# Performance work log

Measured on AMD Instinct MI355X. Metric: run time of the kernel, lower is better.

Reference implementation:

```python
import jax, jax.numpy as jnp
import numpy as np

SQRT2 = 1.4142135623730951  # ScaleCostWeight(sqrt(2)) applied to residuals
N_ITERS = 10
DAMP = 1e-8  # tiny Tikhonov for numerical safety of the 6x6 solve


def _hat(phi):
    x, y, z = phi[0], phi[1], phi[2]
    o = jnp.zeros((), phi.dtype)
    return jnp.stack([jnp.stack([o, -z, y]),
                      jnp.stack([z, o, -x]),
                      jnp.stack([-y, x, o])])


def se3_exp(xi):
    # xi: [6] = [rho (trans), phi (rot)] -> 4x4 SE3 matrix
    rho, phi = xi[:3], xi[3:]
    theta2 = jnp.sum(phi * phi)
    small = theta2 < 1e-12
    theta2s = jnp.where(small, 1.0, theta2)  # double-where for safe grads
    theta = jnp.sqrt(theta2s)
    A = jnp.where(small, 1.0, jnp.sin(theta) / theta)
    B = jnp.where(small, 0.5, (1.0 - jnp.cos(theta)) / theta2s)
    C = jnp.where(small, 1.0 / 6.0, (theta - jnp.sin(theta)) / (theta2s * theta))
    K = _hat(phi)
    K2 = K @ K
    I3 = jnp.eye(3, dtype=xi.dtype)
    R = I3 + A * K + B * K2
    V = I3 + B * K + C * K2
    t = V @ rho
    top = jnp.concatenate([R, t[:, None]], axis=1)
    bot = jnp.array([[0.0, 0.0, 0.0, 1.0]], dtype=xi.dtype)
    return jnp.concatenate([top, bot], axis=0)


def se3_inv(T):
    R = T[..., :3, :3]
    t = T[..., :3, 3:]
    Rt = jnp.swapaxes(R, -1, -2)
    top = jnp.concatenate([Rt, -(Rt @ t)], axis=-1)
    bot = jnp.broadcast_to(jnp.array([0.0, 0.0, 0.0, 1.0], T.dtype),
                           T.shape[:-2] + (1, 4))
    return jnp.concatenate([top, bot], axis=-2)


def _r_single(xi, T, src3, trg3, Wh, w):
    # residual of one batch element at local perturbation xi (retract on right)
    Tn = T @ se3_exp(xi)
    pred = Tn[:3, :3] @ src3 + Tn[:3, 3:4]          # [3, N]
    e = trg3 - pred                                  # [3, N]
    ew = jnp.einsum('nij,jn->in', Wh, e) * w         # cholesky-weighted, w: [1,N]
    return (ew * SQRT2).reshape(-1)                  # [3N]


def _forward(src4, trg4, w, T_init, inv_cov, T_s_v):
    src3 = src4[:, :3, :]
    trg3 = trg4[:, :3, :]
    # W_half = cholesky(inv_cov)^T, computed once (aux var, constant over iters)
    Wh = jnp.swapaxes(jnp.linalg.cholesky(inv_cov), -1, -2)  # [B, N, 3, 3]
    B = src4.shape[0]
    I6 = jnp.eye(6, dtype=src4.dtype)

    def step(T, _):
        xi0 = jnp.zeros((B, 6), T.dtype)
        J = jax.vmap(jax.jacfwd(_r_single), in_axes=(0, 0, 0, 0, 0, 0))(
            xi0, T, src3, trg3, Wh, w)               # [B, 3N, 6]
        r = jax.vmap(_r_single)(xi0, T, src3, trg3, Wh, w)  # [B, 3N]
        g = jnp.einsum('bri,br->bi', J, r)
        H = jnp.einsum('bri,brj->bij', J, J) + DAMP * I6
        dx = -jnp.linalg.solve(H, g[..., None])[..., 0]
        return T @ jax.vmap(se3_exp)(dx), None

    T, _ = jax.lax.scan(step, T_init, None, length=N_ITERS)
    T_sv = jnp.broadcast_to(T_s_v, (B, 4, 4))
    return se3_inv(T_sv) @ T @ T_sv


def setup_inputs() -> dict:
    key = jax.random.key(0)
    B, N = 256, 2048
    k1, k2, k3, k4, k5, k6 = jax.random.split(key, 6)
    src3 = 2.0 * jax.random.normal(k1, (B, 3, N), dtype=jnp.float32)
    # well-posed registration problem: trg = T_true * src + noise
    T_true = jax.vmap(se3_exp)(0.3 * jax.random.normal(k2, (B, 6), dtype=jnp.float32))
    trg3 = (jnp.einsum('bij,bjn->bin', T_true[:, :3, :3], src3)
            + T_true[:, :3, 3:4]
            + 0.01 * jax.random.normal(k3, (B, 3, N), dtype=jnp.float32))
    ones = jnp.ones((B, 1, N), dtype=jnp.float32)
    keypoints_3D_src = jnp.concatenate([src3, ones], axis=1)
    keypoints_3D_trg = jnp.concatenate([trg3, ones], axis=1)
    weights = jax.random.uniform(k4, (B, 1, N), dtype=jnp.float32,
                                 minval=0.1, maxval=1.0)
    A = 0.3 * jax.random.normal(k5, (B, N, 3, 3), dtype=jnp.float32)
    inv_cov_weights = A @ jnp.swapaxes(A, -1, -2) + jnp.eye(3, dtype=jnp.float32)
    T_trg_src_init = jax.vmap(se3_exp)(
        0.05 * jax.random.normal(k6, (B, 6), dtype=jnp.float32))
    T_s_v = se3_exp(jnp.array([0.1, -0.2, 0.3, 0.2, -0.1, 0.15], dtype=jnp.float32))
    return {"keypoints_3D_src": keypoints_3D_src,
            "keypoints_3D_trg": keypoints_3D_trg,
            "weights": weights,
            "T_trg_src_init": T_trg_src_init,
            "inv_cov_weights": inv_cov_weights,
            "T_s_v": T_s_v}


def reference(keypoints_3D_src, keypoints_3D_trg, weights, T_trg_src_init,
              inv_cov_weights, T_s_v):
    return _forward(keypoints_3D_src, keypoints_3D_trg, weights,
                    T_trg_src_init, inv_cov_weights, T_s_v)
```

## Files before the change

kernel.cpp:

```cpp
#include <hip/hip_runtime.h>
#include <math.h>

#define NPTS   2048
#define BD1    256
#define PPT    (NPTS / BD1)
#define NMOM   72
#define NITERS 10
#define DAMPF  1e-8f

__launch_bounds__(BD1, 1)
__global__ void moments_kernel(const float* __restrict__ src4,
                               const float* __restrict__ trg4,
                               const float* __restrict__ wts,
                               const float* __restrict__ icov,
                               float* __restrict__ mom, int B)
{
    const int b   = blockIdx.x;
    const int tid = threadIdx.x;

    const float* srcb = src4 + (size_t)b * 4 * NPTS;
    const float* trgb = trg4 + (size_t)b * 4 * NPTS;
    const float* wb   = wts  + (size_t)b * NPTS;
    const float* cb   = icov + (size_t)b * NPTS * 9;

    float acc[NMOM];
    #pragma unroll
    for (int k = 0; k < NMOM; ++k) acc[k] = 0.0f;

    #pragma unroll
    for (int kk = 0; kk < PPT; ++kk) {
        int n = tid + kk * BD1;
        float sx = srcb[n], sy = srcb[NPTS + n], sz = srcb[2 * NPTS + n];
        float gx = trgb[n], gy = trgb[NPTS + n], gz = trgb[2 * NPTS + n];
        float w  = wb[n];
        const float* c = cb + (size_t)n * 9;
        float w2 = 2.0f * w * w;
        float W[6];
        W[0] = w2 * c[0];
        W[1] = w2 * c[3];
        W[2] = w2 * c[6];
        W[3] = w2 * c[4];
        W[4] = w2 * c[7];
        W[5] = w2 * c[8];

        float hx = W[0] * gx + W[1] * gy + W[2] * gz;
        float hy = W[1] * gx + W[3] * gy + W[4] * gz;
        float hz = W[2] * gx + W[4] * gy + W[5] * gz;

        float sv[3] = { sx, sy, sz };
        float hv[3] = { hx, hy, hz };
        float ss[6] = { sx*sx, sx*sy, sx*sz, sy*sy, sy*sz, sz*sz };

        #pragma unroll
        for (int ij = 0; ij < 6; ++ij) {
            acc[ij] += W[ij];
            #pragma unroll
            for (int c2 = 0; c2 < 3; ++c2) acc[6 + ij * 3 + c2] += W[ij] * sv[c2];
            #pragma unroll
            for (int cd = 0; cd < 6; ++cd) acc[24 + ij * 6 + cd] += W[ij] * ss[cd];
        }
        acc[60] += hx; acc[61] += hy; acc[62] += hz;
        #pragma unroll
        for (int c2 = 0; c2 < 3; ++c2)
            #pragma unroll
            for (int i = 0; i < 3; ++i) acc[63 + c2 * 3 + i] += sv[c2] * hv[i];
    }

    __shared__ float lds[36][BD1 + 1];
    #pragma unroll
    for (int h = 0; h < 2; ++h) {
        if (h) __syncthreads();
        #pragma unroll
        for (int k = 0; k < 36; ++k) lds[k][tid] = acc[h * 36 + k];
        __syncthreads();
        if (tid < 36) {
            const float* row = lds[tid];
            float s0 = 0.f, s1 = 0.f, s2 = 0.f, s3 = 0.f;
            #pragma unroll 8
            for (int j = 0; j < BD1; j += 4) {
                s0 += row[j]; s1 += row[j + 1]; s2 += row[j + 2]; s3 += row[j + 3];
            }
            mom[(h * 36 + tid) * B + b] = (s0 + s1) + (s2 + s3);
        }
    }
}

__launch_bounds__(64, 1)
__global__ void solve_kernel(const float* __restrict__ mom,
                             const float* __restrict__ Tinit,
                             const float* __restrict__ Tsv,
                             float* __restrict__ out, int B)
{
    const int b = blockIdx.x * 64 + threadIdx.x;
    if (b >= B) return;

    float m[NMOM];
    #pragma unroll
    for (int k = 0; k < NMOM; ++k) m[k] = mom[k * B + b];

    float Rm[3][3], tv[3];
    #pragma unroll
    for (int i = 0; i < 3; ++i) {
        #pragma unroll
        for (int j = 0; j < 3; ++j) Rm[i][j] = Tinit[b * 16 + i * 4 + j];
        tv[i] = Tinit[b * 16 + i * 4 + 3];
    }

    const int SY[3][3] = { {0,1,2}, {1,3,4}, {2,4,5} };

    for (int it = 0; it < NITERS; ++it) {
        float C1[6][3];
        #pragma unroll
        for (int ij = 0; ij < 6; ++ij) {
            float a0 = m[6 + ij * 3 + 0], a1 = m[6 + ij * 3 + 1], a2 = m[6 + ij * 3 + 2];
            #pragma unroll
            for (int a = 0; a < 3; ++a)
                C1[ij][a] = Rm[a][0] * a0 + Rm[a][1] * a1 + Rm[a][2] * a2;
        }
        float SM[3][3], SWp[3];
        #pragma unroll
        for (int i = 0; i < 3; ++i) {
            SM[i][0] = C1[SY[i][1]][2] - C1[SY[i][2]][1];
            SM[i][1] = C1[SY[i][2]][0] - C1[SY[i][0]][2];
            SM[i][2] = C1[SY[i][0]][1] - C1[SY[i][1]][0];
            SWp[i]   = C1[SY[i][0]][0] + C1[SY[i][1]][1] + C1[SY[i][2]][2];
        }
        float P2[6][6];
        #pragma unroll
        for (int ij = 0; ij < 6; ++ij) {
            float S00 = m[24 + ij * 6 + 0], S01 = m[24 + ij * 6 + 1], S02 = m[24 + ij * 6 + 2];
            float S11 = m[24 + ij * 6 + 3], S12 = m[24 + ij * 6 + 4], S22 = m[24 + ij * 6 + 5];
            float U[3][3];
            #pragma unroll
            for (int a = 0; a < 3; ++a) {
                U[a][0] = Rm[a][0] * S00 + Rm[a][1] * S01 + Rm[a][2] * S02;
                U[a][1] = Rm[a][0] * S01 + Rm[a][1] * S11 + Rm[a][2] * S12;
                U[a][2] = Rm[a][0] * S02 + Rm[a][1] * S12 + Rm[a][2] * S22;
            }
            P2[0][ij] = U[0][0]*Rm[0][0] + U[0][1]*Rm[0][1] + U[0][2]*Rm[0][2];
            P2[1][ij] = U[0][0]*Rm[1][0] + U[0][1]*Rm[1][1] + U[0][2]*Rm[1][2];
            P2[2][ij] = U[0][0]*Rm[2][0] + U[0][1]*Rm[2][1] + U[0][2]*Rm[2][2];
            P2[3][ij] = U[1][0]*Rm[1][0] + U[1][1]*Rm[1][1] + U[1][2]*Rm[1][2];
            P2[4][ij] = U[1][0]*Rm[2][0] + U[1][1]*Rm[2][1] + U[1][2]*Rm[2][2];
            P2[5][ij] = U[2][0]*Rm[2][0] + U[2][1]*Rm[2][1] + U[2][2]*Rm[2][2];
        }
        float SN00 = -P2[5][3] + 2.f * P2[4][4] - P2[3][5];
        float SN01 = -P2[2][4] + P2[5][1] + P2[1][5] - P2[4][2];
        float SN02 = -P2[4][1] + P2[2][3] + P2[3][2] - P2[1][4];
        float SN11 =  2.f * P2[2][2] - P2[5][0] - P2[0][5];
        float SN12 =  P2[4][0] - P2[2][1] - P2[1][2] + P2[0][4];
        float SN22 = -P2[3][0] + 2.f * P2[1][1] - P2[0][3];

        float SWt0 = m[0]*tv[0] + m[1]*tv[1] + m[2]*tv[2];
        float SWt1 = m[1]*tv[0] + m[3]*tv[1] + m[4]*tv[2];
        float SWt2 = m[2]*tv[0] + m[4]*tv[1] + m[5]*tv[2];
        float Su[3] = { m[60] - SWp[0] - SWt0,
                        m[61] - SWp[1] - SWt1,
                        m[62] - SWp[2] - SWt2 };

        float G[3][3];
        #pragma unroll
        for (int a = 0; a < 3; ++a)
            #pragma unroll
            for (int bb = 0; bb < 3; ++bb)
                G[a][bb] = Rm[a][0]*m[63 + 0 + bb] + Rm[a][1]*m[63 + 3 + bb] + Rm[a][2]*m[63 + 6 + bb];
        float ch[3] = { G[1][2] - G[2][1], G[2][0] - G[0][2], G[0][1] - G[1][0] };
        float pw[3];
        pw[0] = P2[1][2] + P2[3][4] + P2[4][5] - P2[2][1] - P2[4][3] - P2[5][4];
        pw[1] = P2[2][0] + P2[4][1] + P2[5][2] - P2[0][2] - P2[1][4] - P2[2][5];
        pw[2] = P2[0][1] + P2[1][3] + P2[2][4] - P2[1][0] - P2[3][1] - P2[4][2];
        float Sq[3];
        #pragma unroll
        for (int i = 0; i < 3; ++i)
            Sq[i] = ch[i] - pw[i] + SM[0][i]*tv[0] + SM[1][i]*tv[1] + SM[2][i]*tv[2];

        float Hm[6][6];
        Hm[0][0] = m[0]; Hm[0][1] = m[1]; Hm[0][2] = m[2];
        Hm[1][1] = m[3]; Hm[1][2] = m[4]; Hm[2][2] = m[5];
        #pragma unroll
        for (int i = 0; i < 3; ++i) {
            Hm[i][3] = -SM[i][0]; Hm[i][4] = -SM[i][1]; Hm[i][5] = -SM[i][2];
        }
        Hm[3][3] = -SN00; Hm[3][4] = -SN01; Hm[3][5] = -SN02;
        Hm[4][4] = -SN11; Hm[4][5] = -SN12; Hm[5][5] = -SN22;
        #pragma unroll
        for (int i = 0; i < 6; ++i) {
            Hm[i][i] += DAMPF;
            #pragma unroll
            for (int j = 0; j < 6; ++j)
                if (j < i) Hm[i][j] = Hm[j][i];
        }
        float rhs[6] = { Su[0], Su[1], Su[2], Sq[0], Sq[1], Sq[2] };

        float L[6][6];
        #pragma unroll
        for (int i = 0; i < 6; ++i) {
            #pragma unroll
            for (int j = 0; j < 6; ++j) {
                if (j > i) continue;
                float sum = Hm[i][j];
                #pragma unroll
                for (int k2 = 0; k2 < 6; ++k2)
                    if (k2 < j) sum -= L[i][k2] * L[j][k2];
                if (i == j) L[i][i] = sqrtf(sum);
                else        L[i][j] = sum / L[j][j];
            }
        }
        float z[6];
        #pragma unroll
        for (int i = 0; i < 6; ++i) {
            float sum = rhs[i];
            #pragma unroll
            for (int k2 = 0; k2 < 6; ++k2)
                if (k2 < i) sum -= L[i][k2] * z[k2];
            z[i] = sum / L[i][i];
        }
        float y[6];
        #pragma unroll
        for (int i = 5; i >= 0; --i) {
            float sum = z[i];
            #pragma unroll
            for (int k2 = 0; k2 < 6; ++k2)
                if (k2 > i) sum -= L[k2][i] * y[k2];
            y[i] = sum / L[i][i];
        }

        float drx = Rm[0][0]*y[0] + Rm[1][0]*y[1] + Rm[2][0]*y[2];
        float dry = Rm[0][1]*y[0] + Rm[1][1]*y[1] + Rm[2][1]*y[2];
        float drz = Rm[0][2]*y[0] + Rm[1][2]*y[1] + Rm[2][2]*y[2];
        float dpx = Rm[0][0]*y[3] + Rm[1][0]*y[4] + Rm[2][0]*y[5];
        float dpy = Rm[0][1]*y[3] + Rm[1][1]*y[4] + Rm[2][1]*y[5];
        float dpz = Rm[0][2]*y[3] + Rm[1][2]*y[4] + Rm[2][2]*y[5];

        float th2  = dpx*dpx + dpy*dpy + dpz*dpz;
        bool  sm   = th2 < 1e-12f;
        float th2s = sm ? 1.0f : th2;
        float th   = sqrtf(th2s);
        float sth  = sinf(th), cth = cosf(th);
        float Ae = sm ? 1.0f : sth / th;
        float Be = sm ? 0.5f : (1.0f - cth) / th2s;
        float Ce = sm ? (1.0f / 6.0f) : (th - sth) / (th2s * th);
        float Rd00 = 1.0f + Be * (dpx*dpx - th2);
        float Rd01 = -Ae * dpz + Be * dpx * dpy;
        float Rd02 =  Ae * dpy + Be * dpx * dpz;
        float Rd10 =  Ae * dpz + Be * dpx * dpy;
        float Rd11 = 1.0f + Be * (dpy*dpy - th2);
        float Rd12 = -Ae * dpx + Be * dpy * dpz;
        float Rd20 = -Ae * dpy + Be * dpx * dpz;
        float Rd21 =  Ae * dpx + Be * dpy * dpz;
        float Rd22 = 1.0f + Be * (dpz*dpz - th2);
        float V00 = 1.0f + Ce * (dpx*dpx - th2);
        float V01 = -Be * dpz + Ce * dpx * dpy;
        float V02 =  Be * dpy + Ce * dpx * dpz;
        float V10 =  Be * dpz + Ce * dpx * dpy;
        float V11 = 1.0f + Ce * (dpy*dpy - th2);
        float V12 = -Be * dpx + Ce * dpy * dpz;
        float V20 = -Be * dpy + Ce * dpx * dpz;
        float V21 =  Be * dpx + Ce * dpy * dpz;
        float V22 = 1.0f + Ce * (dpz*dpz - th2);
        float tdx = V00 * drx + V01 * dry + V02 * drz;
        float tdy = V10 * drx + V11 * dry + V12 * drz;
        float tdz = V20 * drx + V21 * dry + V22 * drz;

        float nR[3][3];
        nR[0][0] = Rm[0][0]*Rd00 + Rm[0][1]*Rd10 + Rm[0][2]*Rd20;
        nR[0][1] = Rm[0][0]*Rd01 + Rm[0][1]*Rd11 + Rm[0][2]*Rd21;
        nR[0][2] = Rm[0][0]*Rd02 + Rm[0][1]*Rd12 + Rm[0][2]*Rd22;
        nR[1][0] = Rm[1][0]*Rd00 + Rm[1][1]*Rd10 + Rm[1][2]*Rd20;
        nR[1][1] = Rm[1][0]*Rd01 + Rm[1][1]*Rd11 + Rm[1][2]*Rd21;
        nR[1][2] = Rm[1][0]*Rd02 + Rm[1][1]*Rd12 + Rm[1][2]*Rd22;
        nR[2][0] = Rm[2][0]*Rd00 + Rm[2][1]*Rd10 + Rm[2][2]*Rd20;
        nR[2][1] = Rm[2][0]*Rd01 + Rm[2][1]*Rd11 + Rm[2][2]*Rd21;
        nR[2][2] = Rm[2][0]*Rd02 + Rm[2][1]*Rd12 + Rm[2][2]*Rd22;
        float ntx = Rm[0][0]*tdx + Rm[0][1]*tdy + Rm[0][2]*tdz + tv[0];
        float nty = Rm[1][0]*tdx + Rm[1][1]*tdy + Rm[1][2]*tdz + tv[1];
        float ntz = Rm[2][0]*tdx + Rm[2][1]*tdy + Rm[2][2]*tdz + tv[2];
        #pragma unroll
        for (int i = 0; i < 3; ++i)
            #pragma unroll
            for (int j = 0; j < 3; ++j) Rm[i][j] = nR[i][j];
        tv[0] = ntx; tv[1] = nty; tv[2] = ntz;
    }

    {
        float R00 = Rm[0][0], R01 = Rm[0][1], R02 = Rm[0][2];
        float R10 = Rm[1][0], R11 = Rm[1][1], R12 = Rm[1][2];
        float R20 = Rm[2][0], R21 = Rm[2][1], R22 = Rm[2][2];
        float tx = tv[0], ty = tv[1], tz = tv[2];

        float Rv00 = Tsv[0], Rv01 = Tsv[1], Rv02 = Tsv[2],  tvx = Tsv[3];
        float Rv10 = Tsv[4], Rv11 = Tsv[5], Rv12 = Tsv[6],  tvy = Tsv[7];
        float Rv20 = Tsv[8], Rv21 = Tsv[9], Rv22 = Tsv[10], tvz = Tsv[11];

        float P00 = R00*Rv00 + R01*Rv10 + R02*Rv20;
        float P01 = R00*Rv01 + R01*Rv11 + R02*Rv21;
        float P02 = R00*Rv02 + R01*Rv12 + R02*Rv22;
        float P10 = R10*Rv00 + R11*Rv10 + R12*Rv20;
        float P11 = R10*Rv01 + R11*Rv11 + R12*Rv21;
        float P12 = R10*Rv02 + R11*Rv12 + R12*Rv22;
        float P20 = R20*Rv00 + R21*Rv10 + R22*Rv20;
        float P21 = R20*Rv01 + R21*Rv11 + R22*Rv21;
        float P22 = R20*Rv02 + R21*Rv12 + R22*Rv22;
        float Ptx = R00*tvx + R01*tvy + R02*tvz + tx;
        float Pty = R10*tvx + R11*tvy + R12*tvz + ty;
        float Ptz = R20*tvx + R21*tvy + R22*tvz + tz;

        float ex = Ptx - tvx, ey = Pty - tvy, ez = Ptz - tvz;
        float* o = out + (size_t)b * 16;
        o[0]  = Rv00*P00 + Rv10*P10 + Rv20*P20;
        o[1]  = Rv00*P01 + Rv10*P11 + Rv20*P21;
        o[2]  = Rv00*P02 + Rv10*P12 + Rv20*P22;
        o[3]  = Rv00*ex  + Rv10*ey  + Rv20*ez;
        o[4]  = Rv01*P00 + Rv11*P10 + Rv21*P20;
        o[5]  = Rv01*P01 + Rv11*P11 + Rv21*P21;
        o[6]  = Rv01*P02 + Rv11*P12 + Rv21*P22;
        o[7]  = Rv01*ex  + Rv11*ey  + Rv21*ez;
        o[8]  = Rv02*P00 + Rv12*P10 + Rv22*P20;
        o[9]  = Rv02*P01 + Rv12*P11 + Rv22*P21;
        o[10] = Rv02*P02 + Rv12*P12 + Rv22*P22;
        o[11] = Rv02*ex  + Rv12*ey  + Rv22*ez;
        o[12] = 0.0f; o[13] = 0.0f; o[14] = 0.0f; o[15] = 1.0f;
    }
}

extern "C" void kernel_launch(void* const* d_in, const int* in_sizes, int n_in,
                              void* d_out, int out_size, void* d_ws, size_t ws_size,
                              hipStream_t stream)
{
    const float* src4  = (const float*)d_in[0];
    const float* trg4  = (const float*)d_in[1];
    const float* wts   = (const float*)d_in[2];
    const float* Tinit = (const float*)d_in[3];
    const float* icov  = (const float*)d_in[4];
    const float* Tsv   = (const float*)d_in[5];

    const int B = in_sizes[3] / 16;
    float* mom = (float*)d_ws;

    hipLaunchKernelGGL(moments_kernel, dim3(B), dim3(BD1), 0, stream,
                       src4, trg4, wts, icov, mom, B);
    hipLaunchKernelGGL(solve_kernel, dim3((B + 63) / 64), dim3(64), 0, stream,
                       mom, Tinit, Tsv, (float*)d_out, B);
}
```

Before: 112.5 us.

## Split point reduction across eight blocks per batch with shuffle-based reduction

The moments kernel now launches eight blocks per batch element, each handling one point per thread. The LDS row-sum reduction is replaced by a butterfly wave shuffle that folds 72 moments down in halves, plus a small shared-memory cross-wave sum, and partial moments are written per chunk. The solve kernel then sums the eight partials. The solve also uses reciprocal-multiplies instead of divides and fast __sinf/__cosf, which trades some accuracy. A redundant duplicate store to o[6] is left in.

Result: slower. 144.9 us (+28.8%).

```diff
diff --git a/kernel.cpp b/kernel.cpp
--- a/kernel.cpp
+++ b/kernel.cpp
@@ -3,85 +3,102 @@
 
 #define NPTS   2048
 #define BD1    256
-#define PPT    (NPTS / BD1)
+#define CH     8
 #define NMOM   72
 #define NITERS 10
 #define DAMPF  1e-8f
 
-__launch_bounds__(BD1, 1)
+__launch_bounds__(BD1, 4)
 __global__ void moments_kernel(const float* __restrict__ src4,
                                const float* __restrict__ trg4,
                                const float* __restrict__ wts,
                                const float* __restrict__ icov,
                                float* __restrict__ mom, int B)
 {
-    const int b   = blockIdx.x;
-    const int tid = threadIdx.x;
+    const int bc   = blockIdx.x;
+    const int b    = bc >> 3;
+    const int c    = bc & 7;
+    const int tid  = threadIdx.x;
+    const int lane = tid & 63;
+    const int wid  = tid >> 6;
+    const int n    = c * BD1 + tid;
 
     const float* srcb = src4 + (size_t)b * 4 * NPTS;
     const float* trgb = trg4 + (size_t)b * 4 * NPTS;
-    const float* wb   = wts  + (size_t)b * NPTS;
-    const float* cb   = icov + (size_t)b * NPTS * 9;
+
+    float sx = srcb[n], sy = srcb[NPTS + n], sz = srcb[2 * NPTS + n];
+    float gx = trgb[n], gy = trgb[NPTS + n], gz = trgb[2 * NPTS + n];
+    float w  = wts[(size_t)b * NPTS + n];
+    const float* cc = icov + ((size_t)b * NPTS + n) * 9;
+    float w2 = 2.0f * w * w;
+    float W[6];
+    W[0] = w2 * cc[0];
+    W[1] = w2 * cc[3];
+    W[2] = w2 * cc[6];
+    W[3] = w2 * cc[4];
+    W[4] = w2 * cc[7];
+    W[5] = w2 * cc[8];
+
+    float hx = W[0] * gx + W[1] * gy + W[2] * gz;
+    float hy = W[1] * gx + W[3] * gy + W[4] * gz;
+    float hz = W[2] * gx + W[4] * gy + W[5] * gz;
+
+    float sv[3] = { sx, sy, sz };
+    float hv[3] = { hx, hy, hz };
+    float ss[6] = { sx*sx, sx*sy, sx*sz, sy*sy, sy*sz, sz*sz };
 
     float acc[NMOM];
     #pragma unroll
-    for (int k = 0; k < NMOM; ++k) acc[k] = 0.0f;
-
-    #pragma unroll
-    for (int kk = 0; kk < PPT; ++kk) {
-        int n = tid + kk * BD1;
-        float sx = srcb[n], sy = srcb[NPTS + n], sz = srcb[2 * NPTS + n];
-        float gx = trgb[n], gy = trgb[NPTS + n], gz = trgb[2 * NPTS + n];
-        float w  = wb[n];
-        const float* c = cb + (size_t)n * 9;
-        float w2 = 2.0f * w * w;
-        float W[6];
-        W[0] = w2 * c[0];
-        W[1] = w2 * c[3];
-        W[2] = w2 * c[6];
-        W[3] = w2 * c[4];
-        W[4] = w2 * c[7];
-        W[5] = w2 * c[8];
-
-        float hx = W[0] * gx + W[1] * gy + W[2] * gz;
-        float hy = W[1] * gx + W[3] * gy + W[4] * gz;
-        float hz = W[2] * gx + W[4] * gy + W[5] * gz;
-
-        float sv[3] = { sx, sy, sz };
-        float hv[3] = { hx, hy, hz };
-        float ss[6] = { sx*sx, sx*sy, sx*sz, sy*sy, sy*sz, sz*sz };
-
-        #pragma unroll
-        for (int ij = 0; ij < 6; ++ij) {
-            acc[ij] += W[ij];
-            #pragma unroll
-            for (int c2 = 0; c2 < 3; ++c2) acc[6 + ij * 3 + c2] += W[ij] * sv[c2];
-            #pragma unroll
-            for (int cd = 0; cd < 6; ++cd) acc[24 + ij * 6 + cd] += W[ij] * ss[cd];
-        }
-        acc[60] += hx; acc[61] += hy; acc[62] += hz;
-        #pragma unroll
-        for (int c2 = 0; c2 < 3; ++c2)
-            #pragma unroll
-            for (int i = 0; i < 3; ++i) acc[63 + c2 * 3 + i] += sv[c2] * hv[i];
-    }
-
-    __shared__ float lds[36][BD1 + 1];
-    #pragma unroll
-    for (int h = 0; h < 2; ++h) {
-        if (h) __syncthreads();
-        #pragma unroll
-        for (int k = 0; k < 36; ++k) lds[k][tid] = acc[h * 36 + k];
-        __syncthreads();
-        if (tid < 36) {
-            const float* row = lds[tid];
-            float s0 = 0.f, s1 = 0.f, s2 = 0.f, s3 = 0.f;
-            #pragma unroll 8
-            for (int j = 0; j < BD1; j += 4) {
-                s0 += row[j]; s1 += row[j + 1]; s2 += row[j + 2]; s3 += row[j + 3];
-            }
-            mom[(h * 36 + tid) * B + b] = (s0 + s1) + (s2 + s3);
-        }
+    for (int ij = 0; ij < 6; ++ij) {
+        acc[ij] = W[ij];
+        #pragma unroll
+        for (int c2 = 0; c2 < 3; ++c2) acc[6 + ij * 3 + c2] = W[ij] * sv[c2];
+        #pragma unroll
+        for (int cd = 0; cd < 6; ++cd) acc[24 + ij * 6 + cd] = W[ij] * ss[cd];
+    }
+    acc[60] = hx; acc[61] = hy; acc[62] = hz;
+    #pragma unroll
+    for (int c2 = 0; c2 < 3; ++c2)
+        #pragma unroll
+        for (int i = 0; i < 3; ++i) acc[63 + c2 * 3 + i] = sv[c2] * hv[i];
+
+    float v36[36];
+    #pragma unroll
+    for (int k = 0; k < 36; ++k) {
+        float lo  = acc[k],  hi  = acc[k + 36];
+        float lox = __shfl_xor(lo, 32, 64);
+        float hix = __shfl_xor(hi, 32, 64);
+        v36[k] = (lane & 32) ? (hi + hix) : (lo + lox);
+    }
+    float v18[18];
+    #pragma unroll
+    for (int k = 0; k < 18; ++k) {
+        float lo  = v36[k],  hi  = v36[k + 18];
+        float lox = __shfl_xor(lo, 16, 64);
+        float hix = __shfl_xor(hi, 16, 64);
+        v18[k] = (lane & 16) ? (hi + hix) : (lo + lox);
+    }
+    #pragma unroll
+    for (int k = 0; k < 18; ++k) {
+        float v = v18[k];
+        v += __shfl_xor(v, 8, 64);
+        v += __shfl_xor(v, 4, 64);
+        v += __shfl_xor(v, 2, 64);
+        v += __shfl_xor(v, 1, 64);
+        v18[k] = v;
+    }
+
+    __shared__ float red[BD1 / 64][NMOM];
+    if ((lane & 15) == 0) {
+        int q = lane >> 4;
+        #pragma unroll
+        for (int k = 0; k < 18; ++k) red[wid][q * 18 + k] = v18[k];
+    }
+    __syncthreads();
+
+    if (tid < NMOM) {
+        float s = red[0][tid] + red[1][tid] + red[2][tid] + red[3][tid];
+        mom[((size_t)tid * CH + c) * B + b] = s;
     }
 }
 
@@ -96,7 +113,12 @@
 
     float m[NMOM];
     #pragma unroll
-    for (int k = 0; k < NMOM; ++k) m[k] = mom[k * B + b];
+    for (int k = 0; k < NMOM; ++k) {
+        float s = 0.0f;
+        #pragma unroll
+        for (int c = 0; c < CH; ++c) s += mom[((size_t)k * CH + c) * B + b];
+        m[k] = s;
+    }
 
     float Rm[3][3], tv[3];
     #pragma unroll
@@ -192,7 +214,7 @@
         }
         float rhs[6] = { Su[0], Su[1], Su[2], Sq[0], Sq[1], Sq[2] };
 
-        float L[6][6];
+        float L[6][6], dinv[6];
         #pragma unroll
         for (int i = 0; i < 6; ++i) {
             #pragma unroll
@@ -202,8 +224,8 @@
                 #pragma unroll
                 for (int k2 = 0; k2 < 6; ++k2)
                     if (k2 < j) sum -= L[i][k2] * L[j][k2];
-                if (i == j) L[i][i] = sqrtf(sum);
-                else        L[i][j] = sum / L[j][j];
+                if (i == j) { L[i][i] = sqrtf(sum); dinv[i] = 1.0f / L[i][i]; }
+                else        L[i][j] = sum * dinv[j];
             }
         }
         float z[6];
@@ -213,7 +235,7 @@
             #pragma unroll
             for (int k2 = 0; k2 < 6; ++k2)
                 if (k2 < i) sum -= L[i][k2] * z[k2];
-            z[i] = sum / L[i][i];
+            z[i] = sum * dinv[i];
         }
         float y[6];
         #pragma unroll
@@ -222,7 +244,7 @@
             #pragma unroll
             for (int k2 = 0; k2 < 6; ++k2)
                 if (k2 > i) sum -= L[k2][i] * y[k2];
-            y[i] = sum / L[i][i];
+            y[i] = sum * dinv[i];
         }
 
         float drx = Rm[0][0]*y[0] + Rm[1][0]*y[1] + Rm[2][0]*y[2];
@@ -236,10 +258,11 @@
         bool  sm   = th2 < 1e-12f;
         float th2s = sm ? 1.0f : th2;
         float th   = sqrtf(th2s);
-        float sth  = sinf(th), cth = cosf(th);
+        float sth  = __sinf(th), cth = __cosf(th);
+        float it2  = 1.0f / th2s;
         float Ae = sm ? 1.0f : sth / th;
-        float Be = sm ? 0.5f : (1.0f - cth) / th2s;
-        float Ce = sm ? (1.0f / 6.0f) : (th - sth) / (th2s * th);
+        float Be = sm ? 0.5f : (1.0f - cth) * it2;
+        float Ce = sm ? (1.0f / 6.0f) : (th - sth) * it2 / th;
         float Rd00 = 1.0f + Be * (dpx*dpx - th2);
         float Rd01 = -Ae * dpz + Be * dpx * dpy;
         float Rd02 =  Ae * dpy + Be * dpx * dpz;
@@ -313,6 +336,7 @@
         o[3]  = Rv00*ex  + Rv10*ey  + Rv20*ez;
         o[4]  = Rv01*P00 + Rv11*P10 + Rv21*P20;
         o[5]  = Rv01*P01 + Rv11*P11 + Rv21*P21;
+        o[6]  = Rv01*P02 + Rv11*P12 + Rv21*P21 + (Rv11*P11 - Rv11*P11);
         o[6]  = Rv01*P02 + Rv11*P12 + Rv21*P22;
         o[7]  = Rv01*ex  + Rv11*ey  + Rv21*ez;
         o[8]  = Rv02*P00 + Rv12*P10 + Rv22*P20;
@@ -337,7 +361,7 @@
     const int B = in_sizes[3] / 16;
     float* mom = (float*)d_ws;
 
-    hipLaunchKernelGGL(moments_kernel, dim3(B), dim3(BD1), 0, stream,
+    hipLaunchKernelGGL(moments_kernel, dim3(B * CH), dim3(BD1), 0, stream,
                        src4, trg4, wts, icov, mom, B);
     hipLaunchKernelGGL(solve_kernel, dim3((B + 63) / 64), dim3(64), 0, stream,
                        mom, Tinit, Tsv, (float*)d_out, B);
```
